# Kernel optimization log

Measured on AMD Instinct MI355X. Metric: run time of the kernel, lower is better.

Reference implementation:

```python
import jax, jax.numpy as jnp
import numpy as np

N = 50000      # nodes
DEG = 16       # avg degree (random edges)
D = 128        # input_dim
H = 128        # hidden_dim
EPS = 1e-12


def setup_inputs() -> dict:
    key = jax.random.key(0)
    kx, ks, kd, kw1, kw2 = jax.random.split(key, 5)
    x = jax.random.normal(kx, (N, D), dtype=jnp.float32)
    src = jax.random.randint(ks, (N * DEG,), 0, N)
    dst = jax.random.randint(kd, (N * DEG,), 0, N)
    loops = jnp.arange(N)  # self-loops (AGNNConv default) -> every node has >=1 in-edge
    edge_index = jnp.stack([jnp.concatenate([src, loops]),
                            jnp.concatenate([dst, loops])]).astype(jnp.int64)
    W1 = jax.random.normal(kw1, (D, H), dtype=jnp.float32) / np.float32(np.sqrt(D))
    b1 = jnp.zeros((H,), dtype=jnp.float32)
    W2 = jax.random.normal(kw2, (H, H), dtype=jnp.float32) / np.float32(np.sqrt(H))
    b2 = jnp.zeros((H,), dtype=jnp.float32)
    beta1 = jnp.ones((), dtype=jnp.float32)
    beta2 = jnp.ones((), dtype=jnp.float32)
    return {"x": x, "edge_index": edge_index, "W1": W1, "b1": b1,
            "beta1": beta1, "W2": W2, "b2": b2, "beta2": beta2}


def _agnn_conv(x, edge_index, W, b, beta):
    n = x.shape[0]
    h = x @ W + b                                   # [N, H] linear projection
    # l2-normalize for cosine similarity
    hn = h * jax.lax.rsqrt(jnp.sum(h * h, axis=-1, keepdims=True) + EPS)
    src, dst = edge_index[0], edge_index[1]
    score = beta * jnp.sum(hn[src] * hn[dst], axis=-1)   # [E] beta * cos(h_i, h_j)
    # segment softmax over incoming edges of each destination node
    m = jax.ops.segment_max(score, dst, num_segments=n)
    e = jnp.exp(score - m[dst])
    denom = jax.ops.segment_sum(e, dst, num_segments=n)
    alpha = e / denom[dst]                               # [E]
    # weighted aggregation of source features
    return jax.ops.segment_sum(alpha[:, None] * h[src], dst, num_segments=n)


def reference(x, edge_index, W1, b1, beta1, W2, b2, beta2):
    h = jax.nn.relu(_agnn_conv(x, edge_index, W1, b1, beta1))
    # dropout (p=0.1) is identity in eval mode
    return jax.nn.relu(_agnn_conv(h, edge_index, W2, b2, beta2))
```

## Files before the change

### kernel.cpp

```cpp
#include <hip/hip_runtime.h>
#include <hip/hip_bf16.h>
#include <hip/hip_fp16.h>


#define FDIM 128
#define SCAN_CHUNK 2048
#define SCAT_EPT 4

typedef _Float16 f16x8 __attribute__((ext_vector_type(8)));
typedef _Float16 f16x2 __attribute__((ext_vector_type(2)));
typedef float f32x4 __attribute__((ext_vector_type(4)));

#if defined(__has_builtin)
#if __has_builtin(__builtin_amdgcn_fdot2)
#define HAS_FDOT2 1
#endif
#endif

__global__ __launch_bounds__(256) void pack_w_kernel(
    const float* __restrict__ W1, const float* __restrict__ W2,
    _Float16* __restrict__ wp1, _Float16* __restrict__ wp2) {
  int t = blockIdx.x * 256 + threadIdx.x;
  const float* W = (t < 2048) ? W1 : W2;
  _Float16* wp   = (t < 2048) ? wp1 : wp2;
  int tt = t & 2047;
  int l = tt & 63, tile = tt >> 6, kt = tile & 3, nt = tile >> 2;
  int kbase = kt * 32 + (l >> 4) * 8, col = nt * 16 + (l & 15);
  f16x8 v;
  #pragma unroll
  for (int j = 0; j < 8; ++j) v[j] = (_Float16)W[(kbase + j) * 128 + col];
  *(f16x8*)(wp + (size_t)tt * 8) = v;
}

template <typename TIN>
__device__ __forceinline__ void mfma_gemm_body(
    const TIN* __restrict__ X, const _Float16* __restrict__ wp,
    const float* __restrict__ bias, __half* __restrict__ H16,
    float* __restrict__ rnorm, int N, int bid) {
  __shared__ _Float16 xt[64][136];
  int tid = threadIdx.x;
  int l = tid & 63, wv = tid >> 6;
  int r0 = bid * 64;

  for (int idx = tid; idx < 64 * 16; idx += 256) {
    int row = idx >> 4, c8 = idx & 15;
    int r = r0 + row; if (r >= N) r = N - 1;
    f16x8 v;
    if constexpr (sizeof(TIN) == 4) {
      const float* px = (const float*)X + (size_t)r * 128 + c8 * 8;
      float4 a = *(const float4*)px;
      float4 b = *(const float4*)(px + 4);
      v[0]=(_Float16)a.x; v[1]=(_Float16)a.y; v[2]=(_Float16)a.z; v[3]=(_Float16)a.w;
      v[4]=(_Float16)b.x; v[5]=(_Float16)b.y; v[6]=(_Float16)b.z; v[7]=(_Float16)b.w;
    } else {
      v = *(const f16x8*)((const __half*)X + (size_t)r * 128 + c8 * 8);
    }
    *(f16x8*)&xt[row][c8 * 8] = v;
  }
  __syncthreads();

  f32x4 acc[8];
  #pragma unroll
  for (int nt = 0; nt < 8; ++nt) acc[nt] = (f32x4){0.f, 0.f, 0.f, 0.f};

  int arow = wv * 16 + (l & 15);
  int koff = (l >> 4) * 8;
  #pragma unroll
  for (int kt = 0; kt < 4; ++kt) {
    f16x8 afrag = *(const f16x8*)&xt[arow][kt * 32 + koff];
    #pragma unroll
    for (int nt = 0; nt < 8; ++nt) {
      f16x8 bfrag = *(const f16x8*)(wp + (size_t)((nt * 4 + kt) * 64 + l) * 8);
      acc[nt] = __builtin_amdgcn_mfma_f32_16x16x32_f16(afrag, bfrag, acc[nt], 0, 0, 0);
    }
  }

  int col = l & 15, g = l >> 4;
  float bv[8];
  #pragma unroll
  for (int nt = 0; nt < 8; ++nt) bv[nt] = bias[nt * 16 + col];

  #pragma unroll
  for (int j = 0; j < 4; ++j) {
    float hv[8]; float s = 0.f;
    #pragma unroll
    for (int nt = 0; nt < 8; ++nt) { hv[nt] = acc[nt][j] + bv[nt]; s += hv[nt] * hv[nt]; }
    s += __shfl_xor(s, 1); s += __shfl_xor(s, 2);
    s += __shfl_xor(s, 4); s += __shfl_xor(s, 8);
    int r = r0 + wv * 16 + g * 4 + j;
    if (r < N) {
      #pragma unroll
      for (int nt = 0; nt < 8; ++nt)
        H16[(size_t)r * 128 + nt * 16 + col] = __float2half(hv[nt]);
      if (col == 0) rnorm[r] = rsqrtf(s + 1e-12f);
    }
  }
}

__device__ __forceinline__ void convert_body(
    const void* __restrict__ ei, int E,
    int* __restrict__ src32, int* __restrict__ dst32,
    int* __restrict__ rank, int* __restrict__ counts, int cbid) {
  const int* eii = (const int*)ei;
  int lane = threadIdx.x & 63;
  int ok = (lane < 32) ? (eii[2 * lane + 1] == 0) : 1;
  bool is64 = (__ballot(ok) == ~0ull);

  int base = (cbid * 256 + threadIdx.x) * 2;
  if (base + 2 <= E) {
    int s0, s1, d0, d1;
    if (is64) {
      const long long* p = (const long long*)ei;
      longlong2 sv = *(const longlong2*)(p + base);
      longlong2 dv = *(const longlong2*)(p + E + base);
      s0 = (int)sv.x; s1 = (int)sv.y; d0 = (int)dv.x; d1 = (int)dv.y;
    } else {
      int2 sv = *(const int2*)(eii + base);
      int2 dv = *(const int2*)(eii + E + base);
      s0 = sv.x; s1 = sv.y; d0 = dv.x; d1 = dv.y;
    }
    int r0 = atomicAdd(&counts[d0], 1);
    int r1 = atomicAdd(&counts[d1], 1);
    *(int2*)(src32 + base) = make_int2(s0, s1);
    *(int2*)(dst32 + base) = make_int2(d0, d1);
    *(int2*)(rank + base)  = make_int2(r0, r1);
  } else {
    for (int e = base; e < E; ++e) {
      int ss, dd;
      if (is64) { const long long* p = (const long long*)ei; ss = (int)p[e]; dd = (int)p[E + e]; }
      else      { ss = eii[e]; dd = eii[E + e]; }
      src32[e] = ss; dst32[e] = dd; rank[e] = atomicAdd(&counts[dd], 1);
    }
  }
}

__global__ __launch_bounds__(256) void convert_gemm1_kernel(
    const void* __restrict__ ei, int E,
    int* __restrict__ src32, int* __restrict__ dst32,
    int* __restrict__ rank, int* __restrict__ counts, int CB,
    const float* __restrict__ X, const _Float16* __restrict__ wp1,
    const float* __restrict__ bias, __half* __restrict__ H16,
    float* __restrict__ rnorm, int N) {
  if ((int)blockIdx.x < CB)
    convert_body(ei, E, src32, dst32, rank, counts, blockIdx.x);
  else
    mfma_gemm_body<float>(X, wp1, bias, H16, rnorm, N, blockIdx.x - CB);
}

__global__ __launch_bounds__(256) void gemm2_kernel(
    const __half* __restrict__ X, const _Float16* __restrict__ wp,
    const float* __restrict__ bias, __half* __restrict__ H16,
    float* __restrict__ rnorm, int N) {
  mfma_gemm_body<__half>(X, wp, bias, H16, rnorm, N, blockIdx.x);
}

__global__ __launch_bounds__(256) void scan_a_kernel(
    const int* __restrict__ counts, int* __restrict__ bsum, int N) {
  __shared__ int ws[4];
  int tid = threadIdx.x;
  int i0 = blockIdx.x * SCAN_CHUNK + tid * 8;
  int s = 0;
  if (i0 + 7 < N) {
    int4 a = *(const int4*)(counts + i0);
    int4 b = *(const int4*)(counts + i0 + 4);
    s = a.x + a.y + a.z + a.w + b.x + b.y + b.z + b.w;
  } else {
    #pragma unroll
    for (int j = 0; j < 8; ++j) if (i0 + j < N) s += counts[i0 + j];
  }
  #pragma unroll
  for (int m = 32; m; m >>= 1) s += __shfl_xor(s, m);
  int lane = tid & 63, wv = tid >> 6;
  if (lane == 0) ws[wv] = s;
  __syncthreads();
  if (tid == 0) bsum[blockIdx.x] = ws[0] + ws[1] + ws[2] + ws[3];
}

__global__ __launch_bounds__(256) void scan_c_kernel(
    const int* __restrict__ counts, const int* __restrict__ bsum,
    int* __restrict__ offsets, int N, int E) {
  __shared__ int wsum[4];
  int tid = threadIdx.x, lane = tid & 63, wv = tid >> 6;

  int bse = 0;
  for (int j = lane; j < (int)blockIdx.x; j += 64) bse += bsum[j];
  #pragma unroll
  for (int m = 32; m; m >>= 1) bse += __shfl_xor(bse, m);

  int i0 = blockIdx.x * SCAN_CHUNK + tid * 8;
  int v[8];
  if (i0 + 7 < N) {
    int4 a = *(const int4*)(counts + i0);
    int4 b = *(const int4*)(counts + i0 + 4);
    v[0]=a.x; v[1]=a.y; v[2]=a.z; v[3]=a.w;
    v[4]=b.x; v[5]=b.y; v[6]=b.z; v[7]=b.w;
  } else {
    #pragma unroll
    for (int j = 0; j < 8; ++j) v[j] = (i0 + j < N) ? counts[i0 + j] : 0;
  }
  int pre[8], t = 0;
  #pragma unroll
  for (int j = 0; j < 8; ++j) { pre[j] = t; t += v[j]; }
  int x = t;
  #pragma unroll
  for (int off = 1; off < 64; off <<= 1) {
    int u = __shfl_up(x, off);
    if (lane >= off) x += u;
  }
  if (lane == 63) wsum[wv] = x;
  __syncthreads();
  int waveoff = 0;
  #pragma unroll
  for (int w = 0; w < 4; ++w) if (w < wv) waveoff += wsum[w];
  int ebase = bse + waveoff + (x - t);
  #pragma unroll
  for (int j = 0; j < 8; ++j) {
    int i = i0 + j;
    if (i < N) offsets[i] = ebase + pre[j];
  }
  if (blockIdx.x == 0 && tid == 0) offsets[N] = E;
}

__global__ __launch_bounds__(256) void scatter_kernel(
    const int* __restrict__ src32, const int* __restrict__ dst32,
    const int* __restrict__ rank, const int* __restrict__ offsets, int E,
    int* __restrict__ csr_src) {
  int base = (blockIdx.x * 256 + threadIdx.x) * SCAT_EPT;
  if (base + SCAT_EPT <= E) {
    int4 s = *(const int4*)(src32 + base);
    int4 d = *(const int4*)(dst32 + base);
    int4 r = *(const int4*)(rank + base);
    int o0 = offsets[d.x], o1 = offsets[d.y], o2 = offsets[d.z], o3 = offsets[d.w];
    csr_src[o0 + r.x] = s.x;
    csr_src[o1 + r.y] = s.y;
    csr_src[o2 + r.z] = s.z;
    csr_src[o3 + r.w] = s.w;
  } else {
    for (int j = 0; j < SCAT_EPT; ++j) {
      int e = base + j; if (e >= E) break;
      csr_src[offsets[dst32[e]] + rank[e]] = src32[e];
    }
  }
}

template <bool OUT_HALF>
__global__ __launch_bounds__(256) void agg_kernel(
    const __half* __restrict__ H16, const float* __restrict__ rnorm,
    const float* __restrict__ beta_p, const int* __restrict__ offsets,
    const int* __restrict__ csr_src, void* __restrict__ Yp, int N) {
  int wid = (blockIdx.x * 256 + threadIdx.x) >> 6;
  int lane = threadIdx.x & 63;
  if (wid >= N) return;
  int g = lane >> 4;
  int l = lane & 15;
  const float4* H4 = (const float4*)H16;

  float4 hdv = H4[(size_t)wid * 16 + l];
  const __half2* hdp = (const __half2*)&hdv;
  float2 d0 = __half22float2(hdp[0]);
  float2 d1 = __half22float2(hdp[1]);
  float2 d2 = __half22float2(hdp[2]);
  float2 d3 = __half22float2(hdp[3]);
  float rdb = rnorm[wid] * beta_p[0];

  int e0 = offsets[wid], e1 = offsets[wid + 1];
  float denom = 0.f;
  float acc[8] = {0.f,0.f,0.f,0.f,0.f,0.f,0.f,0.f};

  int eA = e0 + g;
  bool vA = eA < e1;
  int sA = vA ? csr_src[eA] : wid;
  float4 hA = H4[(size_t)sA * 16 + l];
  float rA = rnorm[sA];

  int eB = eA + 4;
  bool vB = eB < e1;
  int sB = vB ? csr_src[eB] : wid;
  float4 hB = H4[(size_t)sB * 16 + l];
  float rB = rnorm[sB];

  for (int eb = e0; eb < e1; eb += 4) {
    int eC = eb + 8 + g;
    bool vC = eC < e1;
    int sC = vC ? csr_src[eC] : wid;
    float4 hC = H4[(size_t)sC * 16 + l];
    float rC = rnorm[sC];

    const __half2* hp = (const __half2*)&hA;
    float2 q0 = __half22float2(hp[0]);
    float2 q1 = __half22float2(hp[1]);
    float2 q2 = __half22float2(hp[2]);
    float2 q3 = __half22float2(hp[3]);
#ifdef HAS_FDOT2
    const f16x2* ha2 = (const f16x2*)&hA;
    const f16x2* hd2 = (const f16x2*)&hdv;
    float p = 0.f;
    #pragma unroll
    for (int t = 0; t < 4; ++t) p = __builtin_amdgcn_fdot2(ha2[t], hd2[t], p, false);
#else
    float p = q0.x*d0.x + q0.y*d0.y + q1.x*d1.x + q1.y*d1.y
            + q2.x*d2.x + q2.y*d2.y + q3.x*d3.x + q3.y*d3.y;
#endif
    p += __shfl_xor(p, 1);
    p += __shfl_xor(p, 2);
    p += __shfl_xor(p, 4);
    p += __shfl_xor(p, 8);
    float w = vA ? __expf(p * rdb * rA) : 0.f;
    denom += w;
    acc[0] += w*q0.x; acc[1] += w*q0.y; acc[2] += w*q1.x; acc[3] += w*q1.y;
    acc[4] += w*q2.x; acc[5] += w*q2.y; acc[6] += w*q3.x; acc[7] += w*q3.y;

    vA = vB; hA = hB; rA = rB;
    vB = vC; hB = hC; rB = rC;
  }

  #pragma unroll
  for (int m = 16; m <= 32; m <<= 1) {
    denom += __shfl_xor(denom, m);
    #pragma unroll
    for (int j = 0; j < 8; ++j) acc[j] += __shfl_xor(acc[j], m);
  }
  if (g == 0) {
    float inv = 1.0f / denom;
    float o[8];
    #pragma unroll
    for (int j = 0; j < 8; ++j) o[j] = fmaxf(acc[j] * inv, 0.f);
    if constexpr (OUT_HALF) {
      float4 pack;
      __half2* hp2 = (__half2*)&pack;
      hp2[0] = __floats2half2_rn(o[0], o[1]);
      hp2[1] = __floats2half2_rn(o[2], o[3]);
      hp2[2] = __floats2half2_rn(o[4], o[5]);
      hp2[3] = __floats2half2_rn(o[6], o[7]);
      ((float4*)Yp)[(size_t)wid * 16 + l] = pack;
    } else {
      float4 o0 = {o[0], o[1], o[2], o[3]};
      float4 o1 = {o[4], o[5], o[6], o[7]};
      ((float4*)Yp)[(size_t)wid * 32 + 2 * l] = o0;
      ((float4*)Yp)[(size_t)wid * 32 + 2 * l + 1] = o1;
    }
  }
}

extern "C" void kernel_launch(void* const* d_in, const int* in_sizes, int n_in,
                              void* d_out, int out_size, void* d_ws, size_t ws_size,
                              hipStream_t stream) {
  const float* x     = (const float*)d_in[0];
  const void*  ei    = d_in[1];
  const float* W1    = (const float*)d_in[2];
  const float* b1    = (const float*)d_in[3];
  const float* beta1 = (const float*)d_in[4];
  const float* W2    = (const float*)d_in[5];
  const float* b2    = (const float*)d_in[6];
  const float* beta2 = (const float*)d_in[7];

  int N = in_sizes[0] / FDIM;
  int E = in_sizes[1] / 2;

  char* p = (char*)d_ws;
  auto alloc = [&](size_t bytes) {
    char* r = p; p += (bytes + 255) & ~size_t(255); return r;
  };
  int*      counts  = (int*)alloc(sizeof(int) * N);
  int*      offsets = (int*)alloc(sizeof(int) * (N + 1));
  int*      bsum    = (int*)alloc(sizeof(int) * 256);
  int*      src32   = (int*)alloc(sizeof(int) * E);
  int*      dst32   = (int*)alloc(sizeof(int) * E);
  int*      rank    = (int*)alloc(sizeof(int) * E);
  int*      csr     = (int*)alloc(sizeof(int) * E);
  __half*   h16     = (__half*)alloc(sizeof(__half) * (size_t)N * FDIM);
  float*    rn      = (float*)alloc(sizeof(float) * N);
  __half*   y1h     = (__half*)alloc(sizeof(__half) * (size_t)N * FDIM);
  _Float16* wp1     = (_Float16*)alloc(sizeof(_Float16) * 2048 * 8);
  _Float16* wp2     = (_Float16*)alloc(sizeof(_Float16) * 2048 * 8);

  hipMemsetAsync(counts, 0, sizeof(int) * N, stream);
  pack_w_kernel<<<16, 256, 0, stream>>>(W1, W2, wp1, wp2);

  int cb  = (E + 511) / 512;
  int gb  = (N + 63) / 64;
  int sb  = (E + 256 * SCAT_EPT - 1) / (256 * SCAT_EPT);
  int nb  = (N + SCAN_CHUNK - 1) / SCAN_CHUNK;
  int ab  = (N + 3) / 4;

  convert_gemm1_kernel<<<cb + gb, 256, 0, stream>>>(
      ei, E, src32, dst32, rank, counts, cb, x, wp1, b1, h16, rn, N);
  scan_a_kernel<<<nb, 256, 0, stream>>>(counts, bsum, N);
  scan_c_kernel<<<nb, 256, 0, stream>>>(counts, bsum, offsets, N, E);
  scatter_kernel<<<sb, 256, 0, stream>>>(src32, dst32, rank, offsets, E, csr);

  agg_kernel<true><<<ab, 256, 0, stream>>>(h16, rn, beta1, offsets, csr, y1h, N);
  gemm2_kernel<<<gb, 256, 0, stream>>>(y1h, wp2, b2, h16, rn, N);
  agg_kernel<false><<<ab, 256, 0, stream>>>(h16, rn, beta2, offsets, csr, d_out, N);
}
```

Measured before the change: 239.1 us.

## Build CSR with two-pass LDS radix bucketing instead of global atomics

Replaces the global per-node atomic counting, scan and scatter CSR build with a two-level radix-style sort. Edges are first bucketed by dst>>8 using shared-memory histograms and a scan over block-by-bin counts, then each bucket is finished locally with LDS atomics that produce both offsets and the CSR. The goal is to avoid contended global atomics and random scattered writes. In exchange it adds extra passes over 8-byte pairs, and gemm1 no longer overlaps with edge conversion in a single fused launch.

```diff
diff --git a/kernel.cpp b/kernel.cpp
--- a/kernel.cpp
+++ b/kernel.cpp
@@ -5,7 +5,7 @@
 
 #define FDIM 128
 #define SCAN_CHUNK 2048
-#define SCAT_EPT 4
+#define K1_CHUNK 4096
 
 typedef _Float16 f16x8 __attribute__((ext_vector_type(8)));
 typedef _Float16 f16x2 __attribute__((ext_vector_type(2)));
@@ -30,6 +30,161 @@
   #pragma unroll
   for (int j = 0; j < 8; ++j) v[j] = (_Float16)W[(kbase + j) * 128 + col];
   *(f16x8*)(wp + (size_t)tt * 8) = v;
+}
+
+__global__ __launch_bounds__(256) void hist_convert_kernel(
+    const void* __restrict__ ei, int E, int NBINS, int NB1,
+    int2* __restrict__ pairs0, int* __restrict__ g_hist) {
+  __shared__ int hist[256];
+  int tid = threadIdx.x;
+  hist[tid] = 0;
+  const int* eii = (const int*)ei;
+  int lane = tid & 63;
+  int ok = (lane < 32) ? (eii[2 * lane + 1] == 0) : 1;
+  bool is64 = (__ballot(ok) == ~0ull);
+  __syncthreads();
+  int base = blockIdx.x * K1_CHUNK;
+  for (int j = 0; j < 16; ++j) {
+    int e = base + j * 256 + tid;
+    if (e < E) {
+      int s, d;
+      if (is64) {
+        const long long* p = (const long long*)ei;
+        s = (int)p[e]; d = (int)p[(size_t)E + e];
+      } else {
+        s = eii[e]; d = eii[E + e];
+      }
+      pairs0[e] = make_int2(d, s);
+      atomicAdd(&hist[d >> 8], 1);
+    }
+  }
+  __syncthreads();
+  if (tid < NBINS) g_hist[tid * NB1 + blockIdx.x] = hist[tid];
+}
+
+__global__ __launch_bounds__(256) void scan_a_kernel(
+    const int* __restrict__ in, int* __restrict__ bsum, int L) {
+  __shared__ int ws[4];
+  int tid = threadIdx.x;
+  int i0 = blockIdx.x * SCAN_CHUNK + tid * 8;
+  int s = 0;
+  if (i0 + 7 < L) {
+    int4 a = *(const int4*)(in + i0);
+    int4 b = *(const int4*)(in + i0 + 4);
+    s = a.x + a.y + a.z + a.w + b.x + b.y + b.z + b.w;
+  } else {
+    #pragma unroll
+    for (int j = 0; j < 8; ++j) if (i0 + j < L) s += in[i0 + j];
+  }
+  #pragma unroll
+  for (int m = 32; m; m >>= 1) s += __shfl_xor(s, m);
+  int lane = tid & 63, wv = tid >> 6;
+  if (lane == 0) ws[wv] = s;
+  __syncthreads();
+  if (tid == 0) bsum[blockIdx.x] = ws[0] + ws[1] + ws[2] + ws[3];
+}
+
+__global__ __launch_bounds__(256) void scan_c_kernel(
+    const int* __restrict__ in, const int* __restrict__ bsum,
+    int* __restrict__ out, int L, int TOT) {
+  __shared__ int wsum[4];
+  int tid = threadIdx.x, lane = tid & 63, wv = tid >> 6;
+
+  int bse = 0;
+  for (int j = lane; j < (int)blockIdx.x; j += 64) bse += bsum[j];
+  #pragma unroll
+  for (int m = 32; m; m >>= 1) bse += __shfl_xor(bse, m);
+
+  int i0 = blockIdx.x * SCAN_CHUNK + tid * 8;
+  int v[8];
+  if (i0 + 7 < L) {
+    int4 a = *(const int4*)(in + i0);
+    int4 b = *(const int4*)(in + i0 + 4);
+    v[0]=a.x; v[1]=a.y; v[2]=a.z; v[3]=a.w;
+    v[4]=b.x; v[5]=b.y; v[6]=b.z; v[7]=b.w;
+  } else {
+    #pragma unroll
+    for (int j = 0; j < 8; ++j) v[j] = (i0 + j < L) ? in[i0 + j] : 0;
+  }
+  int pre[8], t = 0;
+  #pragma unroll
+  for (int j = 0; j < 8; ++j) { pre[j] = t; t += v[j]; }
+  int x = t;
+  #pragma unroll
+  for (int off = 1; off < 64; off <<= 1) {
+    int u = __shfl_up(x, off);
+    if (lane >= off) x += u;
+  }
+  if (lane == 63) wsum[wv] = x;
+  __syncthreads();
+  int waveoff = 0;
+  #pragma unroll
+  for (int w = 0; w < 4; ++w) if (w < wv) waveoff += wsum[w];
+  int ebase = bse + waveoff + (x - t);
+  #pragma unroll
+  for (int j = 0; j < 8; ++j) {
+    int i = i0 + j;
+    if (i < L) out[i] = ebase + pre[j];
+  }
+  if (blockIdx.x == 0 && tid == 0) out[L] = TOT;
+}
+
+__global__ __launch_bounds__(256) void radix_scatter_kernel(
+    const int2* __restrict__ pairs0, const int* __restrict__ g_scan,
+    int E, int NBINS, int NB1, int2* __restrict__ pairs1) {
+  __shared__ int cur[256];
+  int tid = threadIdx.x;
+  if (tid < NBINS) cur[tid] = g_scan[tid * NB1 + blockIdx.x];
+  __syncthreads();
+  int base = blockIdx.x * K1_CHUNK;
+  for (int j = 0; j < 16; ++j) {
+    int e = base + j * 256 + tid;
+    if (e < E) {
+      int2 pr = pairs0[e];
+      int pos = atomicAdd(&cur[pr.x >> 8], 1);
+      pairs1[pos] = pr;
+    }
+  }
+}
+
+__global__ __launch_bounds__(256) void bucket_csr_kernel(
+    const int2* __restrict__ pairs1, const int* __restrict__ g_scan,
+    int N, int NB1, int E, int* __restrict__ offsets, int* __restrict__ csr) {
+  __shared__ int hist[256];
+  __shared__ int cur[256];
+  __shared__ int wsum[4];
+  int tid = threadIdx.x, lane = tid & 63, wv = tid >> 6;
+  int b = blockIdx.x;
+  int segbase = g_scan[(size_t)b * NB1];
+  int segend  = g_scan[(size_t)(b + 1) * NB1];
+  hist[tid] = 0;
+  __syncthreads();
+  for (int i = segbase + tid; i < segend; i += 256)
+    atomicAdd(&hist[pairs1[i].x & 255], 1);
+  __syncthreads();
+  int v = hist[tid];
+  int x = v;
+  #pragma unroll
+  for (int off = 1; off < 64; off <<= 1) {
+    int u = __shfl_up(x, off);
+    if (lane >= off) x += u;
+  }
+  if (lane == 63) wsum[wv] = x;
+  __syncthreads();
+  int waveoff = 0;
+  #pragma unroll
+  for (int w = 0; w < 4; ++w) if (w < wv) waveoff += wsum[w];
+  int excl = segbase + waveoff + (x - v);
+  int dglob = b * 256 + tid;
+  if (dglob < N) offsets[dglob] = excl;
+  cur[tid] = excl;
+  if (b == 0 && tid == 0) offsets[N] = E;
+  __syncthreads();
+  for (int i = segbase + tid; i < segend; i += 256) {
+    int2 pr = pairs1[i];
+    int pos = atomicAdd(&cur[pr.x & 255], 1);
+    csr[pos] = pr.y;
+  }
 }
 
 template <typename TIN>
@@ -97,54 +252,11 @@
   }
 }
 
-__device__ __forceinline__ void convert_body(
-    const void* __restrict__ ei, int E,
-    int* __restrict__ src32, int* __restrict__ dst32,
-    int* __restrict__ rank, int* __restrict__ counts, int cbid) {
-  const int* eii = (const int*)ei;
-  int lane = threadIdx.x & 63;
-  int ok = (lane < 32) ? (eii[2 * lane + 1] == 0) : 1;
-  bool is64 = (__ballot(ok) == ~0ull);
-
-  int base = (cbid * 256 + threadIdx.x) * 2;
-  if (base + 2 <= E) {
-    int s0, s1, d0, d1;
-    if (is64) {
-      const long long* p = (const long long*)ei;
-      longlong2 sv = *(const longlong2*)(p + base);
-      longlong2 dv = *(const longlong2*)(p + E + base);
-      s0 = (int)sv.x; s1 = (int)sv.y; d0 = (int)dv.x; d1 = (int)dv.y;
-    } else {
-      int2 sv = *(const int2*)(eii + base);
-      int2 dv = *(const int2*)(eii + E + base);
-      s0 = sv.x; s1 = sv.y; d0 = dv.x; d1 = dv.y;
-    }
-    int r0 = atomicAdd(&counts[d0], 1);
-    int r1 = atomicAdd(&counts[d1], 1);
-    *(int2*)(src32 + base) = make_int2(s0, s1);
-    *(int2*)(dst32 + base) = make_int2(d0, d1);
-    *(int2*)(rank + base)  = make_int2(r0, r1);
-  } else {
-    for (int e = base; e < E; ++e) {
-      int ss, dd;
-      if (is64) { const long long* p = (const long long*)ei; ss = (int)p[e]; dd = (int)p[E + e]; }
-      else      { ss = eii[e]; dd = eii[E + e]; }
-      src32[e] = ss; dst32[e] = dd; rank[e] = atomicAdd(&counts[dd], 1);
-    }
-  }
-}
-
-__global__ __launch_bounds__(256) void convert_gemm1_kernel(
-    const void* __restrict__ ei, int E,
-    int* __restrict__ src32, int* __restrict__ dst32,
-    int* __restrict__ rank, int* __restrict__ counts, int CB,
-    const float* __restrict__ X, const _Float16* __restrict__ wp1,
+__global__ __launch_bounds__(256) void gemm1_kernel(
+    const float* __restrict__ X, const _Float16* __restrict__ wp,
     const float* __restrict__ bias, __half* __restrict__ H16,
     float* __restrict__ rnorm, int N) {
-  if ((int)blockIdx.x < CB)
-    convert_body(ei, E, src32, dst32, rank, counts, blockIdx.x);
-  else
-    mfma_gemm_body<float>(X, wp1, bias, H16, rnorm, N, blockIdx.x - CB);
+  mfma_gemm_body<float>(X, wp, bias, H16, rnorm, N, blockIdx.x);
 }
 
 __global__ __launch_bounds__(256) void gemm2_kernel(
@@ -152,95 +264,6 @@
     const float* __restrict__ bias, __half* __restrict__ H16,
     float* __restrict__ rnorm, int N) {
   mfma_gemm_body<__half>(X, wp, bias, H16, rnorm, N, blockIdx.x);
-}
-
-__global__ __launch_bounds__(256) void scan_a_kernel(
-    const int* __restrict__ counts, int* __restrict__ bsum, int N) {
-  __shared__ int ws[4];
-  int tid = threadIdx.x;
-  int i0 = blockIdx.x * SCAN_CHUNK + tid * 8;
-  int s = 0;
-  if (i0 + 7 < N) {
-    int4 a = *(const int4*)(counts + i0);
-    int4 b = *(const int4*)(counts + i0 + 4);
-    s = a.x + a.y + a.z + a.w + b.x + b.y + b.z + b.w;
-  } else {
-    #pragma unroll
-    for (int j = 0; j < 8; ++j) if (i0 + j < N) s += counts[i0 + j];
-  }
-  #pragma unroll
-  for (int m = 32; m; m >>= 1) s += __shfl_xor(s, m);
-  int lane = tid & 63, wv = tid >> 6;
-  if (lane == 0) ws[wv] = s;
-  __syncthreads();
-  if (tid == 0) bsum[blockIdx.x] = ws[0] + ws[1] + ws[2] + ws[3];
-}
-
-__global__ __launch_bounds__(256) void scan_c_kernel(
-    const int* __restrict__ counts, const int* __restrict__ bsum,
-    int* __restrict__ offsets, int N, int E) {
-  __shared__ int wsum[4];
-  int tid = threadIdx.x, lane = tid & 63, wv = tid >> 6;
-
-  int bse = 0;
-  for (int j = lane; j < (int)blockIdx.x; j += 64) bse += bsum[j];
-  #pragma unroll
-  for (int m = 32; m; m >>= 1) bse += __shfl_xor(bse, m);
-
-  int i0 = blockIdx.x * SCAN_CHUNK + tid * 8;
-  int v[8];
-  if (i0 + 7 < N) {
-    int4 a = *(const int4*)(counts + i0);
-    int4 b = *(const int4*)(counts + i0 + 4);
-    v[0]=a.x; v[1]=a.y; v[2]=a.z; v[3]=a.w;
-    v[4]=b.x; v[5]=b.y; v[6]=b.z; v[7]=b.w;
-  } else {
-    #pragma unroll
-    for (int j = 0; j < 8; ++j) v[j] = (i0 + j < N) ? counts[i0 + j] : 0;
-  }
-  int pre[8], t = 0;
-  #pragma unroll
-  for (int j = 0; j < 8; ++j) { pre[j] = t; t += v[j]; }
-  int x = t;
-  #pragma unroll
-  for (int off = 1; off < 64; off <<= 1) {
-    int u = __shfl_up(x, off);
-    if (lane >= off) x += u;
-  }
-  if (lane == 63) wsum[wv] = x;
-  __syncthreads();
-  int waveoff = 0;
-  #pragma unroll
-  for (int w = 0; w < 4; ++w) if (w < wv) waveoff += wsum[w];
-  int ebase = bse + waveoff + (x - t);
-  #pragma unroll
-  for (int j = 0; j < 8; ++j) {
-    int i = i0 + j;
-    if (i < N) offsets[i] = ebase + pre[j];
-  }
-  if (blockIdx.x == 0 && tid == 0) offsets[N] = E;
-}
-
-__global__ __launch_bounds__(256) void scatter_kernel(
-    const int* __restrict__ src32, const int* __restrict__ dst32,
-    const int* __restrict__ rank, const int* __restrict__ offsets, int E,
-    int* __restrict__ csr_src) {
-  int base = (blockIdx.x * 256 + threadIdx.x) * SCAT_EPT;
-  if (base + SCAT_EPT <= E) {
-    int4 s = *(const int4*)(src32 + base);
-    int4 d = *(const int4*)(dst32 + base);
-    int4 r = *(const int4*)(rank + base);
-    int o0 = offsets[d.x], o1 = offsets[d.y], o2 = offsets[d.z], o3 = offsets[d.w];
-    csr_src[o0 + r.x] = s.x;
-    csr_src[o1 + r.y] = s.y;
-    csr_src[o2 + r.z] = s.z;
-    csr_src[o3 + r.w] = s.w;
-  } else {
-    for (int j = 0; j < SCAT_EPT; ++j) {
-      int e = base + j; if (e >= E) break;
-      csr_src[offsets[dst32[e]] + rank[e]] = src32[e];
-    }
-  }
 }
 
 template <bool OUT_HALF>
@@ -357,38 +380,39 @@
   int N = in_sizes[0] / FDIM;
   int E = in_sizes[1] / 2;
 
+  int NBINS = (N + 255) / 256;
+  int NB1   = (E + K1_CHUNK - 1) / K1_CHUNK;
+  int L2    = NBINS * NB1;
+
   char* p = (char*)d_ws;
   auto alloc = [&](size_t bytes) {
     char* r = p; p += (bytes + 255) & ~size_t(255); return r;
   };
-  int*      counts  = (int*)alloc(sizeof(int) * N);
+  int*      g_hist  = (int*)alloc(sizeof(int) * L2);
+  int*      g_scan  = (int*)alloc(sizeof(int) * (L2 + 1));
+  int*      bsum    = (int*)alloc(sizeof(int) * 64);
+  int2*     pairs0  = (int2*)alloc(sizeof(int2) * E);
+  int2*     pairs1  = (int2*)alloc(sizeof(int2) * E);
+  int*      csr     = (int*)alloc(sizeof(int) * E);
   int*      offsets = (int*)alloc(sizeof(int) * (N + 1));
-  int*      bsum    = (int*)alloc(sizeof(int) * 256);
-  int*      src32   = (int*)alloc(sizeof(int) * E);
-  int*      dst32   = (int*)alloc(sizeof(int) * E);
-  int*      rank    = (int*)alloc(sizeof(int) * E);
-  int*      csr     = (int*)alloc(sizeof(int) * E);
   __half*   h16     = (__half*)alloc(sizeof(__half) * (size_t)N * FDIM);
   float*    rn      = (float*)alloc(sizeof(float) * N);
   __half*   y1h     = (__half*)alloc(sizeof(__half) * (size_t)N * FDIM);
   _Float16* wp1     = (_Float16*)alloc(sizeof(_Float16) * 2048 * 8);
   _Float16* wp2     = (_Float16*)alloc(sizeof(_Float16) * 2048 * 8);
 
-  hipMemsetAsync(counts, 0, sizeof(int) * N, stream);
+  int nb2 = (L2 + SCAN_CHUNK - 1) / SCAN_CHUNK;
+  int gb  = (N + 63) / 64;
+  int ab  = (N + 3) / 4;
+
   pack_w_kernel<<<16, 256, 0, stream>>>(W1, W2, wp1, wp2);
-
-  int cb  = (E + 511) / 512;
-  int gb  = (N + 63) / 64;
-  int sb  = (E + 256 * SCAT_EPT - 1) / (256 * SCAT_EPT);
-  int nb  = (N + SCAN_CHUNK - 1) / SCAN_CHUNK;
-  int ab  = (N + 3) / 4;
-
-  convert_gemm1_kernel<<<cb + gb, 256, 0, stream>>>(
-      ei, E, src32, dst32, rank, counts, cb, x, wp1, b1, h16, rn, N);
-  scan_a_kernel<<<nb, 256, 0, stream>>>(counts, bsum, N);
-  scan_c_kernel<<<nb, 256, 0, stream>>>(counts, bsum, offsets, N, E);
-  scatter_kernel<<<sb, 256, 0, stream>>>(src32, dst32, rank, offsets, E, csr);
-
+  hist_convert_kernel<<<NB1, 256, 0, stream>>>(ei, E, NBINS, NB1, pairs0, g_hist);
+  scan_a_kernel<<<nb2, 256, 0, stream>>>(g_hist, bsum, L2);
+  scan_c_kernel<<<nb2, 256, 0, stream>>>(g_hist, bsum, g_scan, L2, E);
+  radix_scatter_kernel<<<NB1, 256, 0, stream>>>(pairs0, g_scan, E, NBINS, NB1, pairs1);
+  bucket_csr_kernel<<<NBINS, 256, 0, stream>>>(pairs1, g_scan, N, NB1, E, offsets, csr);
+
+  gemm1_kernel<<<gb, 256, 0, stream>>>(x, wp1, b1, h16, rn, N);
   agg_kernel<true><<<ab, 256, 0, stream>>>(h16, rn, beta1, offsets, csr, y1h, N);
   gemm2_kernel<<<gb, 256, 0, stream>>>(y1h, wp2, b2, h16, rn, N);
   agg_kernel<false><<<ab, 256, 0, stream>>>(h16, rn, beta2, offsets, csr, d_out, N);
```

Result: faster. 217.3 us (-9.1%).
